# Performance work log

Measured on AMD Instinct MI355X. Metric: run time of the kernel, lower is better.

The kernel has to match this reference:

```python
import jax, jax.numpy as jnp
import numpy as np

B, S, H = 2, 2048, 1024
NH = 16
HD = H // NH  # 64


def _linear_params(key, fan_in, fan_out):
    k1, k2 = jax.random.split(key)
    bound = 1.0 / np.sqrt(fan_in)
    W = jax.random.uniform(k1, (fan_in, fan_out), jnp.float32, -bound, bound)
    b = jax.random.uniform(k2, (fan_out,), jnp.float32, -bound, bound)
    return W, b


def setup_inputs() -> dict:
    key = jax.random.key(0)
    ks = jax.random.split(key, 7)
    hidden_states = jax.random.normal(ks[0], (B, S, H), jnp.float32)
    governance_embeddings = jax.random.normal(ks[1], (B, H), jnp.float32)
    Wq, bq = _linear_params(ks[2], H, H)
    Wk, bk = _linear_params(ks[3], H, H)
    Wv, bv = _linear_params(ks[4], H, H)
    Wgq, bgq = _linear_params(ks[5], H, H)
    Wgk, bgk = _linear_params(ks[6], H, H)
    return {
        'hidden_states': hidden_states,
        'governance_embeddings': governance_embeddings,
        'Wq': Wq, 'bq': bq, 'Wk': Wk, 'bk': bk, 'Wv': Wv, 'bv': bv,
        'Wgq': Wgq, 'bgq': bgq, 'Wgk': Wgk, 'bgk': bgk,
    }


def reference(hidden_states, governance_embeddings, Wq, bq, Wk, bk, Wv, bv, Wgq, bgq, Wgk, bgk):
    b, s, h = hidden_states.shape
    # QKV projections -> [b, nh, s, hd]
    def heads(x):
        return x.reshape(b, s, NH, HD).transpose(0, 2, 1, 3)
    q = heads(hidden_states @ Wq + bq)
    k = heads(hidden_states @ Wk + bk)
    v = heads(hidden_states @ Wv + bv)

    scale = jnp.float32(1.0 / np.sqrt(HD))
    scores = jnp.einsum('bhid,bhjd->bhij', q, k) * scale  # [b,nh,s,s]

    # governance bias: one query per example vs per-token keys (unscaled)
    gq = (governance_embeddings @ Wgq + bgq).reshape(b, NH, HD)      # [b,nh,hd]
    gk = (hidden_states @ Wgk + bgk).reshape(b, s, NH, HD)           # [b,s,nh,hd]
    gov_scores = jnp.einsum('bhd,bshd->bhs', gq, gk)                 # [b,nh,s]

    # bias is constant along key dim (torch expand on last axis)
    combined = scores + 0.1 * gov_scores[..., :, None]

    probs = jax.nn.softmax(combined, axis=-1)  # dropout = identity (eval)
    context = jnp.einsum('bhij,bhjd->bhid', probs, v)
    context = context.transpose(0, 2, 1, 3).reshape(b, s, h)

    entropy = -jnp.sum(probs * jnp.log(probs + 1e-8), axis=-1).mean()
    influence = jnp.abs(gov_scores).mean()  # mean over expanded tensor == mean over [b,nh,s]
    concentration = probs.max(axis=-1).mean()
    return context, entropy, influence, concentration
```

## Files before the change

### kernel.cpp

```cpp
#include <hip/hip_runtime.h>


typedef unsigned short u16;
typedef __attribute__((ext_vector_type(8))) short bf16x8;
typedef __attribute__((ext_vector_type(4))) float f32x4;
typedef __attribute__((ext_vector_type(16))) float f32x16;
typedef __attribute__((ext_vector_type(4))) u16 u16x4;
typedef __attribute__((ext_vector_type(4))) float float4v;
typedef __attribute__((ext_vector_type(2))) unsigned uint2v;

typedef const __attribute__((address_space(1))) void gvoid_t;
typedef __attribute__((address_space(3))) void lvoid_t;

__device__ __forceinline__ void gl_lds16(const void* g, void* l) {
  __builtin_amdgcn_global_load_lds((gvoid_t*)g, (lvoid_t*)l, 16, 0, 0);
}

__device__ __forceinline__ u16 f2bf(float x) {
  union { float f; unsigned u; } v; v.f = x;
  unsigned r = v.u + 0x7fffu + ((v.u >> 16) & 1u);
  return (u16)(r >> 16);
}
__device__ __forceinline__ float bf2f(u16 h) {
  union { unsigned u; float f; } v; v.u = ((unsigned)h) << 16; return v.f;
}
__device__ __forceinline__ unsigned pk2(float hi, float lo) {
  union { float f; unsigned u; } a, b; a.f = hi; b.f = lo;
  return __builtin_amdgcn_perm(a.u, b.u, 0x07060302u);
}
__device__ __forceinline__ bf16x8 mk8(unsigned a, unsigned b, unsigned c, unsigned d) {
  union { unsigned u[4]; bf16x8 v; } x;
  x.u[0] = a; x.u[1] = b; x.u[2] = c; x.u[3] = d; return x.v;
}

#if defined(__has_builtin)
#if __has_builtin(__builtin_amdgcn_permlane32_swap)
#define HAVE_PLSWAP 1
#endif
#endif

__device__ __forceinline__ void plswap(unsigned& a, unsigned& b, int lane) {
#ifdef HAVE_PLSWAP
  uint2v r = __builtin_amdgcn_permlane32_swap(a, b, false, false);
  a = r.x; b = r.y;
#else
  unsigned ca = __builtin_amdgcn_ds_bpermute((lane ^ 32) << 2, a);
  unsigned cb = __builtin_amdgcn_ds_bpermute((lane ^ 32) << 2, b);
  unsigned na = (lane < 32) ? a : cb;
  unsigned nb = (lane < 32) ? ca : b;
  a = na; b = nb;
#endif
}

__global__ void prep(const float* __restrict__ hs,
                     const float* __restrict__ W0, const float* __restrict__ W1,
                     const float* __restrict__ W2, const float* __restrict__ W3,
                     const float* __restrict__ ge, const float* __restrict__ Wgq,
                     u16* __restrict__ hsB, u16* __restrict__ WB,
                     float* __restrict__ gq_part) {
  __shared__ __align__(16) u16 T[64][72];
  int bx = blockIdx.x, tid = threadIdx.x;
  if (bx < 2048) {
    int i = bx * 256 + tid;
    const float4v* in4 = (const float4v*)hs;
    float4v a = in4[i * 2], b = in4[i * 2 + 1];
    bf16x8 v;
    v[0] = (short)f2bf(a.x); v[1] = (short)f2bf(a.y);
    v[2] = (short)f2bf(a.z); v[3] = (short)f2bf(a.w);
    v[4] = (short)f2bf(b.x); v[5] = (short)f2bf(b.y);
    v[6] = (short)f2bf(b.z); v[7] = (short)f2bf(b.w);
    *(bf16x8*)&hsB[(size_t)i * 8] = v;
    return;
  }
  if (bx < 3072) {
    int idx = bx - 2048;
    int mat = idx >> 8, sub = idx & 255;
    const float* W = (mat == 0) ? W0 : (mat == 1) ? W1 : (mat == 2) ? W2 : W3;
    int k0 = (sub >> 4) * 64, n0 = (sub & 15) * 64;
#pragma unroll
    for (int p = 0; p < 4; ++p) {
      int chunk = p * 256 + tid;
      int row = chunk >> 4, cp = chunk & 15;
      float4v v = *(const float4v*)&W[(size_t)(k0 + row) * 1024 + n0 + cp * 4];
      u16x4 o; o.x = f2bf(v.x); o.y = f2bf(v.y); o.z = f2bf(v.z); o.w = f2bf(v.w);
      *(u16x4*)&T[row][cp * 4] = o;
    }
    __syncthreads();
#pragma unroll
    for (int p = 0; p < 2; ++p) {
      int chunk = p * 256 + tid;
      int nrow = chunk >> 3, cp = chunk & 7;
      bf16x8 v;
#pragma unroll
      for (int e = 0; e < 8; ++e) v[e] = (short)T[cp * 8 + e][nrow];
      *(bf16x8*)&WB[(size_t)(mat * 1024 + n0 + nrow) * 1024 + k0 + cp * 8] = v;
    }
    return;
  }
  {
    int idx = bx - 3072;
    int kb = idx >> 1, b = idx & 1;
    int col0 = tid * 4;
    float4v s = {0.f, 0.f, 0.f, 0.f};
    for (int k = kb * 32; k < kb * 32 + 32; ++k) {
      float g = ge[b * 1024 + k];
      float4v w = *(const float4v*)&Wgq[(size_t)k * 1024 + col0];
      s.x += g * w.x; s.y += g * w.y; s.z += g * w.z; s.w += g * w.w;
    }
    *(float4v*)&gq_part[(size_t)idx * 1024 + col0] = s;
  }
}

__global__ __launch_bounds__(256, 3) void gemm_qkvg(
    const u16* __restrict__ A, const u16* __restrict__ Bw,
    const float* __restrict__ bq, const float* __restrict__ bk,
    const float* __restrict__ bv, const float* __restrict__ bgk,
    const float* __restrict__ bgq, const float* __restrict__ gq_part,
    u16* __restrict__ Qb, u16* __restrict__ Kb,
    u16* __restrict__ GKb, u16* __restrict__ Vt,
    float* __restrict__ gq_final, float* __restrict__ acc3) {
  if (blockIdx.x == 1024) {
    int tid = threadIdx.x;
    if (tid < 3) acc3[tid] = 0.f;
#pragma unroll
    for (int i = 0; i < 8; ++i) {
      int t = tid + i * 256;
      float s = bgq[t & 1023];
      for (int kb = 0; kb < 32; ++kb)
        s += gq_part[(size_t)(kb * 2 + (t >> 10)) * 1024 + (t & 1023)];
      gq_final[t] = s;
    }
    return;
  }
  __shared__ __align__(16) u16 As[128 * 32];
  __shared__ __align__(16) u16 Bs[128 * 32];
  const int tid = threadIdx.x, lane = tid & 63, wv = tid >> 6;
  const int li = lane & 15, quad = lane >> 4;
  const int bid = blockIdx.x;
  const int nb = bid & 31, mb = bid >> 5;
  const u16* Ap = A + (size_t)(mb * 128) * 1024;
  const u16* Bp = Bw + (size_t)(nb * 128) * 1024;
  const int wm0 = (wv >> 1) * 64, wn0 = (wv & 1) * 64;

  f32x4 acc[4][4];
#pragma unroll
  for (int t = 0; t < 4; ++t)
#pragma unroll
    for (int u = 0; u < 4; ++u) acc[t][u] = (f32x4){0.f, 0.f, 0.f, 0.f};

  for (int kt = 0; kt < 32; ++kt) {
    __syncthreads();
#pragma unroll
    for (int jj = 0; jj < 2; ++jj) {
      int j = wv * 2 + jj;
      int row = j * 16 + (lane >> 2);
      int co = lane & 3;
      gl_lds16(Ap + (size_t)row * 1024 + kt * 32 + co * 8, &As[j * 512]);
      gl_lds16(Bp + (size_t)row * 1024 + kt * 32 + co * 8, &Bs[j * 512]);
    }
    __syncthreads();
    bf16x8 af[4], bf[4];
#pragma unroll
    for (int t = 0; t < 4; ++t)
      af[t] = *(const bf16x8*)&As[(wm0 + t * 16 + li) * 32 + quad * 8];
#pragma unroll
    for (int u = 0; u < 4; ++u)
      bf[u] = *(const bf16x8*)&Bs[(wn0 + u * 16 + li) * 32 + quad * 8];
#pragma unroll
    for (int t = 0; t < 4; ++t)
#pragma unroll
      for (int u = 0; u < 4; ++u)
        acc[t][u] = __builtin_amdgcn_mfma_f32_16x16x32_bf16(af[t], bf[u], acc[t][u], 0, 0, 0);
  }

  const int nbase = nb * 128;
  const int mat = nbase >> 10;
  if (mat == 2) {
#pragma unroll
    for (int t = 0; t < 4; ++t)
#pragma unroll
      for (int u = 0; u < 4; ++u) {
        int col = (nbase & 1023) + wn0 + u * 16 + li;
        float bb = bv[col];
        int row = mb * 128 + wm0 + t * 16 + quad * 4;
        int b = row >> 11, s = row & 2047;
        uint2 w;
        w.x = pk2(acc[t][u][1] + bb, acc[t][u][0] + bb);
        w.y = pk2(acc[t][u][3] + bb, acc[t][u][2] + bb);
        *(uint2*)&Vt[(size_t)b * (1024 * 2048) + (size_t)col * 2048 + s] = w;
      }
  } else {
    const float* bias = (mat == 0) ? bq : (mat == 1) ? bk : bgk;
    u16* outp = (mat == 0) ? Qb : (mat == 1) ? Kb : GKb;
    const float qscale = (mat == 0) ? 0.18033688f : 1.0f;
#pragma unroll
    for (int t = 0; t < 4; ++t)
#pragma unroll
      for (int u = 0; u < 4; ++u) {
        int col = (nbase & 1023) + wn0 + u * 16 + li;
        float bb = bias[col];
#pragma unroll
        for (int r = 0; r < 4; ++r) {
          int row = mb * 128 + wm0 + t * 16 + quad * 4 + r;
          outp[(size_t)row * 1024 + col] = f2bf((acc[t][u][r] + bb) * qscale);
        }
      }
  }
}

__global__ __launch_bounds__(256, 2) void attn_kernel(
    const u16* __restrict__ Qb, const u16* __restrict__ Kb,
    const u16* __restrict__ Vt, float* __restrict__ out,
    float* __restrict__ acc3 ) {
  __shared__ __align__(16) u16 Ks[2][128 * 64];
  __shared__ __align__(16) u16 Vs[2][64 * 128];
  __shared__ float red[8];

  const int tid = threadIdx.x, lane = tid & 63, wv = tid >> 6;
  const int q_l = lane & 31, half = lane >> 5;
  const int bx = blockIdx.x;
  const int bh = bx & 31, qb = bx >> 5;
  const int b = bh >> 4, h = bh & 15;

  const u16* Qp = Qb + (size_t)(b * 2048 + qb * 128 + wv * 32 + q_l) * 1024 + h * 64;
  const u16* Kp = Kb + (size_t)(b * 2048) * 1024 + h * 64;
  const u16* Vp = Vt + (size_t)b * (1024 * 2048) + (size_t)(h * 64) * 2048;

  bf16x8 qf[4];
#pragma unroll
  for (int s = 0; s < 4; ++s)
    qf[s] = *(const bf16x8*)&Qp[s * 16 + half * 8];

  float m_st = -3.0e38f, l_st = 0.f, e_st = 0.f;
  f32x16 accO[2];
#pragma unroll
  for (int dt = 0; dt < 2; ++dt)
#pragma unroll
    for (int r = 0; r < 16; ++r) accO[dt][r] = 0.f;

#pragma unroll
  for (int jj = 0; jj < 4; ++jj) {
    int j = wv * 4 + jj;
    int row = j * 8 + (lane >> 3);
    int c16 = (lane & 7) ^ (row & 7);
    gl_lds16(Kp + (size_t)row * 1024 + c16 * 8, &Ks[0][j * 512]);
  }
#pragma unroll
  for (int jj = 0; jj < 4; ++jj) {
    int j = wv * 4 + jj;
    int row = j * 4 + (lane >> 4);
    int c16 = (lane & 15) ^ (row & 7);
    gl_lds16(Vp + (size_t)row * 2048 + c16 * 8, &Vs[0][j * 512]);
  }

  for (int kt = 0; kt < 16; ++kt) {
    const int cur = kt & 1;
    __syncthreads();
    if (kt < 15) {
      const u16* Kpt = Kp + (size_t)((kt + 1) * 128) * 1024;
#pragma unroll
      for (int jj = 0; jj < 4; ++jj) {
        int j = wv * 4 + jj;
        int row = j * 8 + (lane >> 3);
        int c16 = (lane & 7) ^ (row & 7);
        gl_lds16(Kpt + (size_t)row * 1024 + c16 * 8, &Ks[cur ^ 1][j * 512]);
      }
#pragma unroll
      for (int jj = 0; jj < 4; ++jj) {
        int j = wv * 4 + jj;
        int row = j * 4 + (lane >> 4);
        int c16 = (lane & 15) ^ (row & 7);
        gl_lds16(Vp + (size_t)row * 2048 + (kt + 1) * 128 + c16 * 8, &Vs[cur ^ 1][j * 512]);
      }
    }
    const u16* KsC = &Ks[cur][0];
    const u16* VsC = &Vs[cur][0];

    float ps = 0.f, es = 0.f, cmx = m_st;
#pragma unroll
    for (int u = 0; u < 4; ++u) {
      f32x16 c;
#pragma unroll
      for (int r = 0; r < 16; ++r) c[r] = 0.f;
#pragma unroll
      for (int s = 0; s < 4; ++s) {
        int p = (2 * s + half) ^ (q_l & 7);
        bf16x8 a = *(const bf16x8*)&KsC[(u * 32 + q_l) * 64 + p * 8];
        c = __builtin_amdgcn_mfma_f32_32x32x16_bf16(a, qf[s], c, 0, 0, 0);
      }
#pragma unroll
      for (int r = 0; r < 16; ++r) {
        float sv = c[r];
        cmx = fmaxf(cmx, sv);
        float pe = exp2f(sv);
        ps += pe;
        es = __builtin_fmaf(pe, sv, es);
        c[r] = pe;
      }
      unsigned p0 = pk2(c[1], c[0]),  p1 = pk2(c[3], c[2]);
      unsigned p2 = pk2(c[5], c[4]),  p3 = pk2(c[7], c[6]);
      unsigned p4 = pk2(c[9], c[8]),  p5 = pk2(c[11], c[10]);
      unsigned p6 = pk2(c[13], c[12]), p7 = pk2(c[15], c[14]);
      plswap(p0, p2, lane); plswap(p1, p3, lane);
      plswap(p4, p6, lane); plswap(p5, p7, lane);
      bf16x8 bf0 = mk8(p0, p1, p2, p3);
      bf16x8 bf1 = mk8(p4, p5, p6, p7);
#pragma unroll
      for (int dt = 0; dt < 2; ++dt) {
        int d = dt * 32 + q_l;
        int pa = (u * 4 + half) ^ (d & 7);
        int pb = (u * 4 + 2 + half) ^ (d & 7);
        bf16x8 av0 = *(const bf16x8*)&VsC[d * 128 + pa * 8];
        accO[dt] = __builtin_amdgcn_mfma_f32_32x32x16_bf16(av0, bf0, accO[dt], 0, 0, 0);
        bf16x8 av1 = *(const bf16x8*)&VsC[d * 128 + pb * 8];
        accO[dt] = __builtin_amdgcn_mfma_f32_32x32x16_bf16(av1, bf1, accO[dt], 0, 0, 0);
      }
    }
    m_st = cmx;
    l_st += ps;
    e_st += es;
  }

  float lsum = l_st + __shfl_xor(l_st, 32, 64);
  float esum = e_st + __shfl_xor(e_st, 32, 64);
  float mm = fmaxf(m_st, __shfl_xor(m_st, 32, 64));
  float inv = 1.0f / lsum;
  float entw = __logf(lsum) - 0.69314718f * esum * inv;
  float concw = exp2f(mm) * inv;

  float* outp = out + (size_t)(b * 2048 + qb * 128 + wv * 32 + q_l) * 1024 + h * 64;
#pragma unroll
  for (int dt = 0; dt < 2; ++dt)
#pragma unroll
    for (int g = 0; g < 4; ++g) {
      float4v o;
      o.x = accO[dt][4 * g + 0] * inv; o.y = accO[dt][4 * g + 1] * inv;
      o.z = accO[dt][4 * g + 2] * inv; o.w = accO[dt][4 * g + 3] * inv;
      *(float4v*)&outp[dt * 32 + 8 * g + 4 * half] = o;
    }

#pragma unroll
  for (int off = 1; off < 64; off <<= 1) {
    entw += __shfl_xor(entw, off, 64);
    concw += __shfl_xor(concw, off, 64);
  }
  if (lane == 0) { red[wv] = entw * 0.5f; red[4 + wv] = concw * 0.5f; }
  __syncthreads();
  if (tid == 0) {
    atomicAdd(&acc3[0], red[0] + red[1] + red[2] + red[3]);
    atomicAdd(&acc3[1], red[4] + red[5] + red[6] + red[7]);
  }
}

__global__ void gov_kernel(const u16* __restrict__ GKb, const float* __restrict__ gq,
                           float* __restrict__ acc_inf) {
  __shared__ float redI[4];
  int lane = threadIdx.x & 63, wv = threadIdx.x >> 6;
  int wid = blockIdx.x * 4 + wv;
  int b = wid >> 11, s = wid & 2047;
  const u16* gk = GKb + (size_t)(b * 2048 + s) * 1024 + lane * 16;
  const float* gqp = gq + b * 1024 + lane * 16;
  bf16x8 g0 = *(const bf16x8*)gk, g1 = *(const bf16x8*)(gk + 8);
  float4v q0 = *(const float4v*)&gqp[0], q1 = *(const float4v*)&gqp[4];
  float4v q2 = *(const float4v*)&gqp[8], q3 = *(const float4v*)&gqp[12];
  float sum = 0.f;
  sum += bf2f((u16)g0[0]) * q0.x + bf2f((u16)g0[1]) * q0.y +
         bf2f((u16)g0[2]) * q0.z + bf2f((u16)g0[3]) * q0.w;
  sum += bf2f((u16)g0[4]) * q1.x + bf2f((u16)g0[5]) * q1.y +
         bf2f((u16)g0[6]) * q1.z + bf2f((u16)g0[7]) * q1.w;
  sum += bf2f((u16)g1[0]) * q2.x + bf2f((u16)g1[1]) * q2.y +
         bf2f((u16)g1[2]) * q2.z + bf2f((u16)g1[3]) * q2.w;
  sum += bf2f((u16)g1[4]) * q3.x + bf2f((u16)g1[5]) * q3.y +
         bf2f((u16)g1[6]) * q3.z + bf2f((u16)g1[7]) * q3.w;
  sum += __shfl_xor(sum, 1, 64);
  sum += __shfl_xor(sum, 2, 64);
  float v = ((lane & 3) == 0) ? fabsf(sum) : 0.f;
  v += __shfl_xor(v, 4, 64);  v += __shfl_xor(v, 8, 64);
  v += __shfl_xor(v, 16, 64); v += __shfl_xor(v, 32, 64);
  if (lane == 0) redI[wv] = v;
  __syncthreads();
  if (threadIdx.x == 0)
    atomicAdd(acc_inf, redI[0] + redI[1] + redI[2] + redI[3]);
}

__global__ void finalize(const float* __restrict__ acc3, float* __restrict__ out) {
  if (threadIdx.x == 0) {
    out[0] = acc3[0] * (1.f / 65536.f);
    out[1] = acc3[2] * (1.f / 65536.f);
    out[2] = acc3[1] * (1.f / 65536.f);
  }
}

extern "C" void kernel_launch(void* const* d_in, const int* in_sizes, int n_in,
                              void* d_out, int out_size, void* d_ws, size_t ws_size,
                              hipStream_t stream) {
  (void)in_sizes; (void)n_in; (void)out_size; (void)ws_size;
  const float* hs  = (const float*)d_in[0];
  const float* ge  = (const float*)d_in[1];
  const float* Wq  = (const float*)d_in[2];
  const float* bq  = (const float*)d_in[3];
  const float* Wk  = (const float*)d_in[4];
  const float* bk  = (const float*)d_in[5];
  const float* Wv  = (const float*)d_in[6];
  const float* bv  = (const float*)d_in[7];
  const float* Wgq = (const float*)d_in[8];
  const float* bgq = (const float*)d_in[9];
  const float* Wgk = (const float*)d_in[10];
  const float* bgk = (const float*)d_in[11];

  char* ws = (char*)d_ws;
  u16* hsB = (u16*)(ws);
  u16* WB  = (u16*)(ws + (size_t)(8 << 20));
  u16* Qb  = (u16*)(ws + (size_t)(16 << 20));
  u16* Kb  = (u16*)(ws + (size_t)(24 << 20));
  u16* Vt  = (u16*)(ws + (size_t)(32 << 20));
  u16* GKb = (u16*)(ws + (size_t)(40 << 20));
  float* gq_part  = (float*)(ws + (size_t)(48 << 20));
  float* gq_final = (float*)(ws + (size_t)(48 << 20) + 262144);
  float* acc3     = (float*)(ws + (size_t)(48 << 20) + 524288);
  float* out = (float*)d_out;

  prep<<<3136, 256, 0, stream>>>(hs, Wq, Wk, Wv, Wgk, ge, Wgq, hsB, WB, gq_part);
  gemm_qkvg<<<1025, 256, 0, stream>>>(hsB, WB, bq, bk, bv, bgk, bgq, gq_part,
                                      Qb, Kb, GKb, Vt, gq_final, acc3);
  attn_kernel<<<512, 256, 0, stream>>>(Qb, Kb, Vt, out, acc3);
  gov_kernel<<<1024, 256, 0, stream>>>(GKb, gq_final, acc3 + 2);
  finalize<<<1, 64, 0, stream>>>(acc3, out + 4194304);
}
```

Before: 232.3 us.

## Double-buffer GEMM LDS tiles and give each attention wave two query tiles

The projection GEMM now uses double-buffered LDS, prefetching the next K-slice while computing the current one, which also drops one barrier per iteration. The attention kernel has each wave handle 64 query rows (two 32-row tiles), so K and V fragments read from LDS are reused across both tiles. The grid shrinks from 512 to 256 blocks. The exp2 call goes to the hardware builtin when available. In exchange, registers per wave roughly double and there are half as many blocks, which may lower occupancy or leave CUs idle on a 256-CU part.

```diff
diff --git a/kernel.cpp b/kernel.cpp
--- a/kernel.cpp
+++ b/kernel.cpp
@@ -37,6 +37,12 @@
 #if __has_builtin(__builtin_amdgcn_permlane32_swap)
 #define HAVE_PLSWAP 1
 #endif
+#if __has_builtin(__builtin_amdgcn_exp2f)
+#define EXP2(x) __builtin_amdgcn_exp2f(x)
+#endif
+#endif
+#ifndef EXP2
+#define EXP2(x) exp2f(x)
 #endif
 
 __device__ __forceinline__ void plswap(unsigned& a, unsigned& b, int lane) {
@@ -132,8 +138,8 @@
     }
     return;
   }
-  __shared__ __align__(16) u16 As[128 * 32];
-  __shared__ __align__(16) u16 Bs[128 * 32];
+  __shared__ __align__(16) u16 As[2][128 * 32];
+  __shared__ __align__(16) u16 Bs[2][128 * 32];
   const int tid = threadIdx.x, lane = tid & 63, wv = tid >> 6;
   const int li = lane & 15, quad = lane >> 4;
   const int bid = blockIdx.x;
@@ -148,24 +154,35 @@
 #pragma unroll
     for (int u = 0; u < 4; ++u) acc[t][u] = (f32x4){0.f, 0.f, 0.f, 0.f};
 
+#pragma unroll
+  for (int jj = 0; jj < 2; ++jj) {
+    int j = wv * 2 + jj;
+    int row = j * 16 + (lane >> 2);
+    int co = lane & 3;
+    gl_lds16(Ap + (size_t)row * 1024 + co * 8, &As[0][j * 512]);
+    gl_lds16(Bp + (size_t)row * 1024 + co * 8, &Bs[0][j * 512]);
+  }
+
   for (int kt = 0; kt < 32; ++kt) {
+    const int cur = kt & 1;
     __syncthreads();
-#pragma unroll
-    for (int jj = 0; jj < 2; ++jj) {
-      int j = wv * 2 + jj;
-      int row = j * 16 + (lane >> 2);
-      int co = lane & 3;
-      gl_lds16(Ap + (size_t)row * 1024 + kt * 32 + co * 8, &As[j * 512]);
-      gl_lds16(Bp + (size_t)row * 1024 + kt * 32 + co * 8, &Bs[j * 512]);
-    }
-    __syncthreads();
+    if (kt < 31) {
+#pragma unroll
+      for (int jj = 0; jj < 2; ++jj) {
+        int j = wv * 2 + jj;
+        int row = j * 16 + (lane >> 2);
+        int co = lane & 3;
+        gl_lds16(Ap + (size_t)row * 1024 + (kt + 1) * 32 + co * 8, &As[cur ^ 1][j * 512]);
+        gl_lds16(Bp + (size_t)row * 1024 + (kt + 1) * 32 + co * 8, &Bs[cur ^ 1][j * 512]);
+      }
+    }
     bf16x8 af[4], bf[4];
 #pragma unroll
     for (int t = 0; t < 4; ++t)
-      af[t] = *(const bf16x8*)&As[(wm0 + t * 16 + li) * 32 + quad * 8];
+      af[t] = *(const bf16x8*)&As[cur][(wm0 + t * 16 + li) * 32 + quad * 8];
 #pragma unroll
     for (int u = 0; u < 4; ++u)
-      bf[u] = *(const bf16x8*)&Bs[(wn0 + u * 16 + li) * 32 + quad * 8];
+      bf[u] = *(const bf16x8*)&Bs[cur][(wn0 + u * 16 + li) * 32 + quad * 8];
 #pragma unroll
     for (int t = 0; t < 4; ++t)
 #pragma unroll
@@ -221,22 +238,27 @@
   const int bx = blockIdx.x;
   const int bh = bx & 31, qb = bx >> 5;
   const int b = bh >> 4, h = bh & 15;
-
-  const u16* Qp = Qb + (size_t)(b * 2048 + qb * 128 + wv * 32 + q_l) * 1024 + h * 64;
+  const int qrow0 = qb * 256 + wv * 64;
+
+  const u16* Qp = Qb + (size_t)(b * 2048 + qrow0 + q_l) * 1024 + h * 64;
   const u16* Kp = Kb + (size_t)(b * 2048) * 1024 + h * 64;
   const u16* Vp = Vt + (size_t)b * (1024 * 2048) + (size_t)(h * 64) * 2048;
 
-  bf16x8 qf[4];
-#pragma unroll
-  for (int s = 0; s < 4; ++s)
-    qf[s] = *(const bf16x8*)&Qp[s * 16 + half * 8];
-
-  float m_st = -3.0e38f, l_st = 0.f, e_st = 0.f;
-  f32x16 accO[2];
-#pragma unroll
-  for (int dt = 0; dt < 2; ++dt)
-#pragma unroll
-    for (int r = 0; r < 16; ++r) accO[dt][r] = 0.f;
+  bf16x8 qf[2][4];
+#pragma unroll
+  for (int qt = 0; qt < 2; ++qt)
+#pragma unroll
+    for (int s = 0; s < 4; ++s)
+      qf[qt][s] = *(const bf16x8*)&Qp[(size_t)qt * 32 * 1024 + s * 16 + half * 8];
+
+  float m_st[2] = {-3.0e38f, -3.0e38f}, l_st[2] = {0.f, 0.f}, e_st[2] = {0.f, 0.f};
+  f32x16 accO[2][2];
+#pragma unroll
+  for (int qt = 0; qt < 2; ++qt)
+#pragma unroll
+    for (int dt = 0; dt < 2; ++dt)
+#pragma unroll
+      for (int r = 0; r < 16; ++r) accO[qt][dt][r] = 0.f;
 
 #pragma unroll
   for (int jj = 0; jj < 4; ++jj) {
@@ -276,69 +298,78 @@
     const u16* KsC = &Ks[cur][0];
     const u16* VsC = &Vs[cur][0];
 
-    float ps = 0.f, es = 0.f, cmx = m_st;
 #pragma unroll
     for (int u = 0; u < 4; ++u) {
-      f32x16 c;
-#pragma unroll
-      for (int r = 0; r < 16; ++r) c[r] = 0.f;
-#pragma unroll
-      for (int s = 0; s < 4; ++s) {
-        int p = (2 * s + half) ^ (q_l & 7);
-        bf16x8 a = *(const bf16x8*)&KsC[(u * 32 + q_l) * 64 + p * 8];
-        c = __builtin_amdgcn_mfma_f32_32x32x16_bf16(a, qf[s], c, 0, 0, 0);
-      }
-#pragma unroll
-      for (int r = 0; r < 16; ++r) {
-        float sv = c[r];
-        cmx = fmaxf(cmx, sv);
-        float pe = exp2f(sv);
-        ps += pe;
-        es = __builtin_fmaf(pe, sv, es);
-        c[r] = pe;
-      }
-      unsigned p0 = pk2(c[1], c[0]),  p1 = pk2(c[3], c[2]);
-      unsigned p2 = pk2(c[5], c[4]),  p3 = pk2(c[7], c[6]);
-      unsigned p4 = pk2(c[9], c[8]),  p5 = pk2(c[11], c[10]);
-      unsigned p6 = pk2(c[13], c[12]), p7 = pk2(c[15], c[14]);
-      plswap(p0, p2, lane); plswap(p1, p3, lane);
-      plswap(p4, p6, lane); plswap(p5, p7, lane);
-      bf16x8 bf0 = mk8(p0, p1, p2, p3);
-      bf16x8 bf1 = mk8(p4, p5, p6, p7);
+      bf16x8 ka[4];
+#pragma unroll
+      for (int s = 0; s < 4; ++s)
+        ka[s] = *(const bf16x8*)&KsC[(u * 32 + q_l) * 64 + (((2 * s + half) ^ (q_l & 7))) * 8];
+      bf16x8 av[2][2];
 #pragma unroll
       for (int dt = 0; dt < 2; ++dt) {
         int d = dt * 32 + q_l;
-        int pa = (u * 4 + half) ^ (d & 7);
-        int pb = (u * 4 + 2 + half) ^ (d & 7);
-        bf16x8 av0 = *(const bf16x8*)&VsC[d * 128 + pa * 8];
-        accO[dt] = __builtin_amdgcn_mfma_f32_32x32x16_bf16(av0, bf0, accO[dt], 0, 0, 0);
-        bf16x8 av1 = *(const bf16x8*)&VsC[d * 128 + pb * 8];
-        accO[dt] = __builtin_amdgcn_mfma_f32_32x32x16_bf16(av1, bf1, accO[dt], 0, 0, 0);
-      }
-    }
-    m_st = cmx;
-    l_st += ps;
-    e_st += es;
-  }
-
-  float lsum = l_st + __shfl_xor(l_st, 32, 64);
-  float esum = e_st + __shfl_xor(e_st, 32, 64);
-  float mm = fmaxf(m_st, __shfl_xor(m_st, 32, 64));
-  float inv = 1.0f / lsum;
-  float entw = __logf(lsum) - 0.69314718f * esum * inv;
-  float concw = exp2f(mm) * inv;
-
-  float* outp = out + (size_t)(b * 2048 + qb * 128 + wv * 32 + q_l) * 1024 + h * 64;
-#pragma unroll
-  for (int dt = 0; dt < 2; ++dt)
-#pragma unroll
-    for (int g = 0; g < 4; ++g) {
-      float4v o;
-      o.x = accO[dt][4 * g + 0] * inv; o.y = accO[dt][4 * g + 1] * inv;
-      o.z = accO[dt][4 * g + 2] * inv; o.w = accO[dt][4 * g + 3] * inv;
-      *(float4v*)&outp[dt * 32 + 8 * g + 4 * half] = o;
-    }
-
+#pragma unroll
+        for (int kc = 0; kc < 2; ++kc)
+          av[dt][kc] = *(const bf16x8*)&VsC[d * 128 + ((u * 4 + kc * 2 + half) ^ (d & 7)) * 8];
+      }
+#pragma unroll
+      for (int qt = 0; qt < 2; ++qt) {
+        f32x16 c;
+#pragma unroll
+        for (int r = 0; r < 16; ++r) c[r] = 0.f;
+#pragma unroll
+        for (int s = 0; s < 4; ++s)
+          c = __builtin_amdgcn_mfma_f32_32x32x16_bf16(ka[s], qf[qt][s], c, 0, 0, 0);
+        float cmx = m_st[qt], ps = 0.f, es = 0.f;
+#pragma unroll
+        for (int r = 0; r < 16; ++r) {
+          float sv = c[r];
+          cmx = fmaxf(cmx, sv);
+          float pe = EXP2(sv);
+          ps += pe;
+          es = __builtin_fmaf(pe, sv, es);
+          c[r] = pe;
+        }
+        m_st[qt] = cmx;
+        l_st[qt] += ps;
+        e_st[qt] += es;
+        unsigned p0 = pk2(c[1], c[0]),   p1 = pk2(c[3], c[2]);
+        unsigned p2 = pk2(c[5], c[4]),   p3 = pk2(c[7], c[6]);
+        unsigned p4 = pk2(c[9], c[8]),   p5 = pk2(c[11], c[10]);
+        unsigned p6 = pk2(c[13], c[12]), p7 = pk2(c[15], c[14]);
+        plswap(p0, p2, lane); plswap(p1, p3, lane);
+        plswap(p4, p6, lane); plswap(p5, p7, lane);
+        bf16x8 bf0 = mk8(p0, p1, p2, p3);
+        bf16x8 bf1 = mk8(p4, p5, p6, p7);
+#pragma unroll
+        for (int dt = 0; dt < 2; ++dt) {
+          accO[qt][dt] = __builtin_amdgcn_mfma_f32_32x32x16_bf16(av[dt][0], bf0, accO[qt][dt], 0, 0, 0);
+          accO[qt][dt] = __builtin_amdgcn_mfma_f32_32x32x16_bf16(av[dt][1], bf1, accO[qt][dt], 0, 0, 0);
+        }
+      }
+    }
+  }
+
+  float entw = 0.f, concw = 0.f;
+#pragma unroll
+  for (int qt = 0; qt < 2; ++qt) {
+    float lsum = l_st[qt] + __shfl_xor(l_st[qt], 32, 64);
+    float esum = e_st[qt] + __shfl_xor(e_st[qt], 32, 64);
+    float mm = fmaxf(m_st[qt], __shfl_xor(m_st[qt], 32, 64));
+    float inv = 1.0f / lsum;
+    entw += __logf(lsum) - 0.69314718f * esum * inv;
+    concw += exp2f(mm) * inv;
+    float* outp = out + (size_t)(b * 2048 + qrow0 + qt * 32 + q_l) * 1024 + h * 64;
+#pragma unroll
+    for (int dt = 0; dt < 2; ++dt)
+#pragma unroll
+      for (int g = 0; g < 4; ++g) {
+        float4v o;
+        o.x = accO[qt][dt][4 * g + 0] * inv; o.y = accO[qt][dt][4 * g + 1] * inv;
+        o.z = accO[qt][dt][4 * g + 2] * inv; o.w = accO[qt][dt][4 * g + 3] * inv;
+        *(float4v*)&outp[dt * 32 + 8 * g + 4 * half] = o;
+      }
+  }
 #pragma unroll
   for (int off = 1; off < 64; off <<= 1) {
     entw += __shfl_xor(entw, off, 64);
@@ -423,7 +454,7 @@
   prep<<<3136, 256, 0, stream>>>(hs, Wq, Wk, Wv, Wgk, ge, Wgq, hsB, WB, gq_part);
   gemm_qkvg<<<1025, 256, 0, stream>>>(hsB, WB, bq, bk, bv, bgk, bgq, gq_part,
                                       Qb, Kb, GKb, Vt, gq_final, acc3);
-  attn_kernel<<<512, 256, 0, stream>>>(Qb, Kb, Vt, out, acc3);
+  attn_kernel<<<256, 256, 0, stream>>>(Qb, Kb, Vt, out, acc3);
   gov_kernel<<<1024, 256, 0, stream>>>(GKb, gq_final, acc3 + 2);
   finalize<<<1, 64, 0, stream>>>(acc3, out + 4194304);
 }
```

New measurement: 292.8 us. 26.0% more time.

## Double-buffer projection GEMM LDS tiles and pack softmax math into float2

Applied to the files above, without the earlier changes.

The projection GEMM now uses two LDS buffers, prefetching the next K-slice while MFMAs run on the current one, and drops one of the two barriers per iteration. This is meant to hide global-to-LDS load latency. In the attention kernel, the softmax exp, sum and entropy accumulation are rewritten with 2-wide float vectors so the compiler can emit packed FP32 ops. exp2f is also replaced with the raw hardware exp2 builtin, skipping denormal and range handling. The cost is double the GEMM LDS footprint and reliance on the single barrier covering the async LDS loads.

```diff
diff --git a/kernel.cpp b/kernel.cpp
--- a/kernel.cpp
+++ b/kernel.cpp
@@ -5,6 +5,7 @@
 typedef __attribute__((ext_vector_type(8))) short bf16x8;
 typedef __attribute__((ext_vector_type(4))) float f32x4;
 typedef __attribute__((ext_vector_type(16))) float f32x16;
+typedef __attribute__((ext_vector_type(2))) float f32x2;
 typedef __attribute__((ext_vector_type(4))) u16 u16x4;
 typedef __attribute__((ext_vector_type(4))) float float4v;
 typedef __attribute__((ext_vector_type(2))) unsigned uint2v;
@@ -37,6 +38,12 @@
 #if __has_builtin(__builtin_amdgcn_permlane32_swap)
 #define HAVE_PLSWAP 1
 #endif
+#if __has_builtin(__builtin_amdgcn_exp2f)
+#define EXP2(x) __builtin_amdgcn_exp2f(x)
+#endif
+#endif
+#ifndef EXP2
+#define EXP2(x) exp2f(x)
 #endif
 
 __device__ __forceinline__ void plswap(unsigned& a, unsigned& b, int lane) {
@@ -132,8 +139,8 @@
     }
     return;
   }
-  __shared__ __align__(16) u16 As[128 * 32];
-  __shared__ __align__(16) u16 Bs[128 * 32];
+  __shared__ __align__(16) u16 As[2][128 * 32];
+  __shared__ __align__(16) u16 Bs[2][128 * 32];
   const int tid = threadIdx.x, lane = tid & 63, wv = tid >> 6;
   const int li = lane & 15, quad = lane >> 4;
   const int bid = blockIdx.x;
@@ -148,24 +155,35 @@
 #pragma unroll
     for (int u = 0; u < 4; ++u) acc[t][u] = (f32x4){0.f, 0.f, 0.f, 0.f};
 
+#pragma unroll
+  for (int jj = 0; jj < 2; ++jj) {
+    int j = wv * 2 + jj;
+    int row = j * 16 + (lane >> 2);
+    int co = lane & 3;
+    gl_lds16(Ap + (size_t)row * 1024 + co * 8, &As[0][j * 512]);
+    gl_lds16(Bp + (size_t)row * 1024 + co * 8, &Bs[0][j * 512]);
+  }
+
   for (int kt = 0; kt < 32; ++kt) {
+    const int cur = kt & 1;
     __syncthreads();
-#pragma unroll
-    for (int jj = 0; jj < 2; ++jj) {
-      int j = wv * 2 + jj;
-      int row = j * 16 + (lane >> 2);
-      int co = lane & 3;
-      gl_lds16(Ap + (size_t)row * 1024 + kt * 32 + co * 8, &As[j * 512]);
-      gl_lds16(Bp + (size_t)row * 1024 + kt * 32 + co * 8, &Bs[j * 512]);
-    }
-    __syncthreads();
+    if (kt < 31) {
+#pragma unroll
+      for (int jj = 0; jj < 2; ++jj) {
+        int j = wv * 2 + jj;
+        int row = j * 16 + (lane >> 2);
+        int co = lane & 3;
+        gl_lds16(Ap + (size_t)row * 1024 + (kt + 1) * 32 + co * 8, &As[cur ^ 1][j * 512]);
+        gl_lds16(Bp + (size_t)row * 1024 + (kt + 1) * 32 + co * 8, &Bs[cur ^ 1][j * 512]);
+      }
+    }
     bf16x8 af[4], bf[4];
 #pragma unroll
     for (int t = 0; t < 4; ++t)
-      af[t] = *(const bf16x8*)&As[(wm0 + t * 16 + li) * 32 + quad * 8];
+      af[t] = *(const bf16x8*)&As[cur][(wm0 + t * 16 + li) * 32 + quad * 8];
 #pragma unroll
     for (int u = 0; u < 4; ++u)
-      bf[u] = *(const bf16x8*)&Bs[(wn0 + u * 16 + li) * 32 + quad * 8];
+      bf[u] = *(const bf16x8*)&Bs[cur][(wn0 + u * 16 + li) * 32 + quad * 8];
 #pragma unroll
     for (int t = 0; t < 4; ++t)
 #pragma unroll
@@ -231,7 +249,7 @@
   for (int s = 0; s < 4; ++s)
     qf[s] = *(const bf16x8*)&Qp[s * 16 + half * 8];
 
-  float m_st = -3.0e38f, l_st = 0.f, e_st = 0.f;
+  f32x2 mx2 = {-3.0e38f, -3.0e38f}, ps2 = {0.f, 0.f}, es2 = {0.f, 0.f};
   f32x16 accO[2];
 #pragma unroll
   for (int dt = 0; dt < 2; ++dt)
@@ -276,7 +294,6 @@
     const u16* KsC = &Ks[cur][0];
     const u16* VsC = &Vs[cur][0];
 
-    float ps = 0.f, es = 0.f, cmx = m_st;
 #pragma unroll
     for (int u = 0; u < 4; ++u) {
       f32x16 c;
@@ -289,17 +306,17 @@
         c = __builtin_amdgcn_mfma_f32_32x32x16_bf16(a, qf[s], c, 0, 0, 0);
       }
 #pragma unroll
-      for (int r = 0; r < 16; ++r) {
-        float sv = c[r];
-        cmx = fmaxf(cmx, sv);
-        float pe = exp2f(sv);
-        ps += pe;
-        es = __builtin_fmaf(pe, sv, es);
-        c[r] = pe;
-      }
-      unsigned p0 = pk2(c[1], c[0]),  p1 = pk2(c[3], c[2]);
-      unsigned p2 = pk2(c[5], c[4]),  p3 = pk2(c[7], c[6]);
-      unsigned p4 = pk2(c[9], c[8]),  p5 = pk2(c[11], c[10]);
+      for (int r = 0; r < 8; ++r) {
+        f32x2 sv = {c[2 * r], c[2 * r + 1]};
+        mx2 = __builtin_elementwise_max(mx2, sv);
+        f32x2 pe = {EXP2(sv.x), EXP2(sv.y)};
+        ps2 += pe;
+        es2 += pe * sv;
+        c[2 * r] = pe.x; c[2 * r + 1] = pe.y;
+      }
+      unsigned p0 = pk2(c[1], c[0]),   p1 = pk2(c[3], c[2]);
+      unsigned p2 = pk2(c[5], c[4]),   p3 = pk2(c[7], c[6]);
+      unsigned p4 = pk2(c[9], c[8]),   p5 = pk2(c[11], c[10]);
       unsigned p6 = pk2(c[13], c[12]), p7 = pk2(c[15], c[14]);
       plswap(p0, p2, lane); plswap(p1, p3, lane);
       plswap(p4, p6, lane); plswap(p5, p7, lane);
@@ -316,17 +333,15 @@
         accO[dt] = __builtin_amdgcn_mfma_f32_32x32x16_bf16(av1, bf1, accO[dt], 0, 0, 0);
       }
     }
-    m_st = cmx;
-    l_st += ps;
-    e_st += es;
-  }
-
+  }
+
+  float l_st = ps2.x + ps2.y, e_st = es2.x + es2.y, m_st = fmaxf(mx2.x, mx2.y);
   float lsum = l_st + __shfl_xor(l_st, 32, 64);
   float esum = e_st + __shfl_xor(e_st, 32, 64);
   float mm = fmaxf(m_st, __shfl_xor(m_st, 32, 64));
   float inv = 1.0f / lsum;
   float entw = __logf(lsum) - 0.69314718f * esum * inv;
-  float concw = exp2f(mm) * inv;
+  float concw = EXP2(mm) * inv;
 
   float* outp = out + (size_t)(b * 2048 + qb * 128 + wv * 32 + q_l) * 1024 + h * 64;
 #pragma unroll
```

Result: faster. 222.5 us (-4.2%).
